# Kernel tuning notes

Hardware: AMD Instinct MI355X
Metric: run time of the kernel (lower is better)

Reference implementation:

```python
import jax, jax.numpy as jnp
import numpy as np

B, D_IN, H, C, K, ND = 65536, 1024, 512, 2, 4, 7
LN_EPS = 1e-5
CE_W = jnp.array([0.1, 0.9], dtype=jnp.float32)


def setup_inputs() -> dict:
    key = jax.random.key(0)
    ks = jax.random.split(key, 12)
    x = jax.random.normal(ks[0], (B, D_IN), dtype=jnp.float32)
    labels = jax.random.randint(ks[1], (B,), 0, C)
    domain = jax.random.randint(ks[2], (B,), 0, ND)
    fc1_w = jax.random.normal(ks[3], (120, D_IN), dtype=jnp.float32) / np.sqrt(D_IN)
    fc1_b = jnp.zeros((120,), dtype=jnp.float32)
    fc2_w = jax.random.normal(ks[4], (H, 120), dtype=jnp.float32) / np.sqrt(120)
    fc2_b = jnp.zeros((H,), dtype=jnp.float32)
    ln_g = jnp.ones((H,), dtype=jnp.float32)
    ln_b = jnp.zeros((H,), dtype=jnp.float32)
    sms = 0.1 * jax.random.normal(ks[5], (K + 1, H, C), dtype=jnp.float32)
    sm_biases = 0.1 * jax.random.normal(ks[6], (K + 1, C), dtype=jnp.float32)
    embs = 1e-4 * jax.random.normal(ks[7], (ND, K), dtype=jnp.float32)
    cs_wt = jnp.asarray(0.1, dtype=jnp.float32) + 1e-4 * jax.random.normal(ks[8], (), dtype=jnp.float32)
    return {"x": x, "labels": labels, "domain": domain, "fc1_w": fc1_w, "fc1_b": fc1_b,
            "fc2_w": fc2_w, "fc2_b": fc2_b, "ln_g": ln_g, "ln_b": ln_b,
            "sms": sms, "sm_biases": sm_biases, "embs": embs, "cs_wt": cs_wt}


def _weighted_ce(logits, labels, w):
    # torch CrossEntropyLoss(weight=w): sum_i w[y_i]*nll_i / sum_i w[y_i]
    logp = jax.nn.log_softmax(logits, axis=-1)
    nll = -jnp.take_along_axis(logp, labels[:, None], axis=1)[:, 0]
    wl = w[labels]
    return jnp.sum(wl * nll) / jnp.sum(wl)


def reference(x, labels, domain, fc1_w, fc1_b, fc2_w, fc2_b, ln_g, ln_b, sms, sm_biases, embs, cs_wt):
    h = jax.nn.relu(x @ fc1_w.T + fc1_b)           # [B,120]
    h = jax.nn.relu(h @ fc2_w.T + fc2_b)           # [B,H]
    mu = jnp.mean(h, axis=-1, keepdims=True)
    var = jnp.var(h, axis=-1, keepdims=True)
    h = (h - mu) / jnp.sqrt(var + LN_EPS) * ln_g + ln_b

    # common classifier (expert 0)
    logits_common = h @ sms[0] + sm_biases[0]      # [B,C]

    # domain mixture weights
    dom1h = jax.nn.one_hot(domain, ND, dtype=jnp.float32)
    c_wts = dom1h @ embs                           # [B,K]
    c_wts = jnp.tanh(jnp.concatenate([jnp.full((h.shape[0], 1), 1.0, jnp.float32) * cs_wt, c_wts], axis=1))  # [B,K+1]

    # reordered einsum chain: K+1 small GEMMs then weighted sum (avoids [B,K+1,H] weight tensor)
    per_k = jnp.einsum('bh,khc->bkc', h, sms)      # [B,K+1,C]
    logits_spec = jnp.einsum('bk,bkc->bc', c_wts, per_k) + c_wts @ sm_biases  # [B,C]

    specific_loss = _weighted_ce(logits_spec, labels, CE_W)
    class_loss = _weighted_ce(logits_common, labels, CE_W)

    # orthogonality penalty: per-class gram of expert weight columns vs identity
    cps = jnp.einsum('khc,jhc->ckj', sms, sms)     # [C,K+1,K+1]
    orth_loss = jnp.mean((cps - jnp.eye(K + 1, dtype=jnp.float32)[None]) ** 2)

    loss = class_loss + specific_loss + orth_loss
    return (loss, logits_common, class_loss, specific_loss, orth_loss)
```

## Files before the change

### kernel.cpp

```cpp
#include <hip/hip_runtime.h>
#include <hip/hip_bf16.h>

typedef __attribute__((ext_vector_type(8))) short short8;
typedef __attribute__((ext_vector_type(4))) float floatx4;
typedef __attribute__((ext_vector_type(8))) unsigned short ushort8;

#define BTOT 65536
#define WS_W1BF   0u
#define WS_W2BF   262144u
#define WS_GBF    393216u
#define WS_CONST  409600u
#define WS_H1BF   524288u
#define WS_PART   17301504u

__device__ __forceinline__ unsigned short f2bf(float f) {
  unsigned u = __float_as_uint(f);
  unsigned r = u + 0x7FFFu + ((u >> 16) & 1u);
  return (unsigned short)(r >> 16);
}

__device__ __forceinline__ void gload16(const void* g, void* l) {
  __builtin_amdgcn_global_load_lds(
      (const __attribute__((address_space(1))) unsigned int*)g,
      (__attribute__((address_space(3))) unsigned int*)l, 16, 0, 0);
}

__global__ __launch_bounds__(256) void k0_prep(
    const float* __restrict__ w1, const float* __restrict__ w2,
    const float* __restrict__ ln_g, const float* __restrict__ ln_b,
    const float* __restrict__ sms, const float* __restrict__ smb,
    const float* __restrict__ embs, const float* __restrict__ cs,
    unsigned char* __restrict__ ws) {
  const int blk = blockIdx.x, tid = threadIdx.x;
  if (blk < 32) {
    for (int g = blk * 256 + tid; g < 16384; g += 32 * 256) {
      int ks = g >> 10, d = g & 1023;
      int n = d >> 3, cp = d & 7, c = cp ^ (n & 7);
      ushort8 u;
      if (n < 120) {
        const float* s = w1 + n * 1024 + ks * 64 + c * 8;
        float4 v0 = *(const float4*)s, v1 = *(const float4*)(s + 4);
        u[0] = f2bf(v0.x); u[1] = f2bf(v0.y); u[2] = f2bf(v0.z); u[3] = f2bf(v0.w);
        u[4] = f2bf(v1.x); u[5] = f2bf(v1.y); u[6] = f2bf(v1.z); u[7] = f2bf(v1.w);
      } else {
#pragma unroll
        for (int j = 0; j < 8; ++j) u[j] = 0;
      }
      *(ushort8*)(ws + WS_W1BF + (unsigned)g * 16) = u;
    }
  } else if (blk < 40) {
    for (int g = (blk - 32) * 256 + tid; g < 8192; g += 8 * 256) {
      int lane = g & 63, f = g >> 6;
      int nt = f & 3, ks = (f >> 2) & 3, w = f >> 4;
      int n = w * 64 + nt * 16 + (lane & 15);
      ushort8 u;
#pragma unroll
      for (int j = 0; j < 8; ++j) {
        int k = ks * 32 + (lane >> 4) * 8 + j;
        u[j] = (k < 120) ? f2bf(w2[n * 120 + k]) : (unsigned short)0;
      }
      *(ushort8*)(ws + WS_W2BF + (unsigned)g * 16) = u;
    }
  } else if (blk == 40) {
    for (int e = tid; e < 1024; e += 256) {
      int t = e >> 6, lane = e & 63, q = lane & 15;
      ushort8 u;
#pragma unroll
      for (int j = 0; j < 8; ++j) {
        int k = t * 32 + (lane >> 4) * 8 + j;
        float v = 0.f;
        if (q < 10) { int kk = q >> 1, c = q & 1; v = ln_g[k] * sms[kk * 1024 + k * 2 + c]; }
        u[j] = f2bf(v);
      }
      *(ushort8*)(ws + WS_GBF + (unsigned)e * 16) = u;
    }
  } else {
    float* cst = (float*)(ws + WS_CONST);
    int lane = tid & 63, w = tid >> 6;
    for (int q = w; q < 10; q += 4) {
      int kk = q >> 1, c = q & 1;
      float s = 0.f;
#pragma unroll
      for (int i = 0; i < 8; ++i) { int k = lane + 64 * i; s += ln_b[k] * sms[kk * 1024 + k * 2 + c]; }
#pragma unroll
      for (int o = 32; o >= 1; o >>= 1) s += __shfl_xor(s, o);
      if (lane == 0) cst[q] = s + smb[kk * 2 + c];
    }
    if (tid == 0) cst[16] = tanhf(cs[0]);
    if (tid < 28) cst[32 + tid] = tanhf(embs[tid]);
  }
}

__global__ __launch_bounds__(512) void k1_gemm1(
    const float* __restrict__ x, const unsigned char* __restrict__ w1bf,
    const float* __restrict__ b1, unsigned char* __restrict__ h1bf) {
  __shared__ unsigned char lds[49152];
  const int tid = threadIdx.x, lane = tid & 63, w = tid >> 6;
  const int l15 = lane & 15, l4 = lane >> 4;
  const long row0 = (long)blockIdx.x * 64;

  const int xr = tid >> 3, xc8 = tid & 7;
  const float* xsrc = x + (row0 + xr) * 1024 + xc8 * 8;
  const unsigned xoff = (unsigned)(xr * 128 + ((xc8 * 16) ^ ((xr & 7) << 4)));
  const unsigned char* wsrc = w1bf + w * 2048 + lane * 16;
  const unsigned wdstoff = 16384u + (unsigned)w * 2048;

  const int col = w * 16 + l15;
  const float bias = (col < 120) ? b1[col] : 0.f;

  floatx4 acc[4];
#pragma unroll
  for (int i = 0; i < 4; ++i) acc[i] = floatx4{0.f, 0.f, 0.f, 0.f};

  float4 v0 = *(const float4*)(xsrc);
  float4 v1 = *(const float4*)(xsrc + 4);
  gload16(wsrc, lds + wdstoff);
  gload16(wsrc + 1024, lds + wdstoff + 1024);
  __builtin_amdgcn_sched_barrier(0);
  {
    ushort8 u;
    u[0] = f2bf(v0.x); u[1] = f2bf(v0.y); u[2] = f2bf(v0.z); u[3] = f2bf(v0.w);
    u[4] = f2bf(v1.x); u[5] = f2bf(v1.y); u[6] = f2bf(v1.z); u[7] = f2bf(v1.w);
    *(ushort8*)(lds + xoff) = u;
  }
  v0 = *(const float4*)(xsrc + 64);
  v1 = *(const float4*)(xsrc + 68);
  __builtin_amdgcn_sched_barrier(0);
  asm volatile("s_waitcnt vmcnt(2) lgkmcnt(0)" ::: "memory");
  __builtin_amdgcn_s_barrier();

  for (int ks = 0; ks < 16; ++ks) {
    const unsigned cur = ks & 1u, nxt = cur ^ 1u;
    if (ks < 15) {
      gload16(wsrc + (ks + 1) * 16384, lds + 16384 + nxt * 16384 + (wdstoff - 16384));
      gload16(wsrc + (ks + 1) * 16384 + 1024, lds + 16384 + nxt * 16384 + (wdstoff - 16384) + 1024);
    }
    __builtin_amdgcn_sched_barrier(0);
    if (ks < 15) {
      ushort8 u;
      u[0] = f2bf(v0.x); u[1] = f2bf(v0.y); u[2] = f2bf(v0.z); u[3] = f2bf(v0.w);
      u[4] = f2bf(v1.x); u[5] = f2bf(v1.y); u[6] = f2bf(v1.z); u[7] = f2bf(v1.w);
      *(ushort8*)(lds + nxt * 8192 + xoff) = u;
    }
    if (ks < 14) {
      v0 = *(const float4*)(xsrc + (ks + 2) * 64);
      v1 = *(const float4*)(xsrc + (ks + 2) * 64 + 4);
    }
    __builtin_amdgcn_sched_barrier(0);
    const unsigned char* Xc = lds + cur * 8192;
    const unsigned char* Wc = lds + 16384 + cur * 16384;
#pragma unroll
    for (int ss = 0; ss < 2; ++ss) {
      short8 a[4];
#pragma unroll
      for (int mt = 0; mt < 4; ++mt) {
        int r = mt * 16 + l15;
        a[mt] = *(const short8*)(Xc + r * 128 + ((ss * 64 + l4 * 16) ^ ((r & 7) << 4)));
      }
      short8 b = *(const short8*)(Wc + col * 128 + ((ss * 64 + l4 * 16) ^ ((col & 7) << 4)));
#pragma unroll
      for (int mt = 0; mt < 4; ++mt)
        acc[mt] = __builtin_amdgcn_mfma_f32_16x16x32_bf16(a[mt], b, acc[mt], 0, 0, 0);
    }
    if (ks < 14) {
      asm volatile("s_waitcnt vmcnt(2) lgkmcnt(0)" ::: "memory");
    } else {
      asm volatile("s_waitcnt vmcnt(0) lgkmcnt(0)" ::: "memory");
    }
    __builtin_amdgcn_s_barrier();
  }

  unsigned char* h1s = lds;
#pragma unroll
  for (int mt = 0; mt < 4; ++mt)
#pragma unroll
    for (int r = 0; r < 4; ++r) {
      int row = mt * 16 + l4 * 4 + r;
      float v = acc[mt][r] + bias;
      v = (col < 120) ? (v > 0.f ? v : 0.f) : 0.f;
      *(unsigned short*)(h1s + row * 256 + ((col * 2) ^ ((row & 7) << 4))) = f2bf(v);
    }
  __syncthreads();
  {
    const unsigned char* s = lds + tid * 32;
    unsigned char* d = h1bf + (long)blockIdx.x * 16384 + tid * 32;
    *(float4*)(d) = *(const float4*)(s);
    *(float4*)(d + 16) = *(const float4*)(s + 16);
  }
}

__global__ __launch_bounds__(512, 4) void k2_fused(
    const unsigned char* __restrict__ h1bf, const unsigned char* __restrict__ w2f,
    const unsigned char* __restrict__ gbf, const float* __restrict__ cst,
    const float* __restrict__ b2, const int* __restrict__ labels,
    const int* __restrict__ domain, float* __restrict__ out,
    float* __restrict__ partials) {
  extern __shared__ unsigned char lds[];
  unsigned char* h1s = lds;
  unsigned char* h2s = lds;
  float* stats = (float*)(lds + 65536);
  float* musig = (float*)(lds + 70656);
  float* Af    = (float*)(lds + 71168);

  const int tid = threadIdx.x, lane = tid & 63, w = tid >> 6;
  const int l15 = lane & 15, l4 = lane >> 4;
  const long row0 = (long)blockIdx.x * 64;
  const int n0 = w * 64;

  {
    const unsigned char* hs = h1bf + (long)blockIdx.x * 16384 + w * 2048 + lane * 16;
    gload16(hs, h1s + w * 2048);
    gload16(hs + 1024, h1s + w * 2048 + 1024);
  }
  float b2v[4];
#pragma unroll
  for (int nt = 0; nt < 4; ++nt) b2v[nt] = b2[n0 + nt * 16 + l15];
  __syncthreads();

  floatx4 acc[4][4];
#pragma unroll
  for (int i = 0; i < 4; ++i)
#pragma unroll
    for (int j = 0; j < 4; ++j) acc[i][j] = floatx4{0.f, 0.f, 0.f, 0.f};
#pragma unroll
  for (int ks = 0; ks < 4; ++ks) {
    short8 a[4], b[4];
#pragma unroll
    for (int nt = 0; nt < 4; ++nt)
      b[nt] = *(const short8*)(w2f + (((w * 4 + ks) * 4 + nt) * 64 + lane) * 16);
#pragma unroll
    for (int mt = 0; mt < 4; ++mt) {
      int r = mt * 16 + l15;
      a[mt] = *(const short8*)(h1s + r * 256 + ((ks * 64 + l4 * 16) ^ ((r & 7) << 4)));
    }
#pragma unroll
    for (int mt = 0; mt < 4; ++mt)
#pragma unroll
      for (int nt = 0; nt < 4; ++nt)
        acc[mt][nt] = __builtin_amdgcn_mfma_f32_16x16x32_bf16(a[mt], b[nt], acc[mt][nt], 0, 0, 0);
  }

#pragma unroll
  for (int mt = 0; mt < 4; ++mt)
#pragma unroll
    for (int nt = 0; nt < 4; ++nt)
#pragma unroll
      for (int r = 0; r < 4; ++r) {
        float v = acc[mt][nt][r] + b2v[nt];
        acc[mt][nt][r] = v > 0.f ? v : 0.f;
      }
#pragma unroll
  for (int mt = 0; mt < 4; ++mt)
#pragma unroll
    for (int r = 0; r < 4; ++r) {
      float s = 0.f, q2 = 0.f;
#pragma unroll
      for (int nt = 0; nt < 4; ++nt) { float v = acc[mt][nt][r]; s += v; q2 += v * v; }
#pragma unroll
      for (int o = 1; o <= 8; o <<= 1) { s += __shfl_xor(s, o); q2 += __shfl_xor(q2, o); }
      if (l15 == 0) {
        int row = mt * 16 + l4 * 4 + r;
        stats[row * 20 + w * 2] = s;
        stats[row * 20 + w * 2 + 1] = q2;
      }
    }
  __syncthreads();

  if (tid < 64) {
    float S = 0.f, Q = 0.f;
#pragma unroll
    for (int j = 0; j < 8; ++j) { S += stats[tid * 20 + j * 2]; Q += stats[tid * 20 + j * 2 + 1]; }
    float mu = S * (1.f / 512.f);
    float var = Q * (1.f / 512.f) - mu * mu;
    musig[tid * 2] = mu;
    musig[tid * 2 + 1] = rsqrtf(var + 1e-5f);
  }
  __syncthreads();

#pragma unroll
  for (int mt = 0; mt < 4; ++mt)
#pragma unroll
    for (int r = 0; r < 4; ++r) {
      int row = mt * 16 + l4 * 4 + r;
      float mu = musig[row * 2], rs = musig[row * 2 + 1];
#pragma unroll
      for (int nt = 0; nt < 4; ++nt) {
        int colc = n0 + nt * 16 + l15;
        float hn = (acc[mt][nt][r] - mu) * rs;
        *(unsigned short*)(h2s + row * 1024 + ((colc * 2) ^ ((row & 7) << 4))) = f2bf(hn);
      }
    }
  __syncthreads();

  if (w < 4) {
    floatx4 a3 = floatx4{0.f, 0.f, 0.f, 0.f};
    int row = w * 16 + l15;
#pragma unroll
    for (int t = 0; t < 16; ++t) {
      short8 aa = *(const short8*)(h2s + row * 1024 + ((t * 64 + l4 * 16) ^ ((row & 7) << 4)));
      short8 bb = *(const short8*)(gbf + t * 1024 + lane * 16);
      a3 = __builtin_amdgcn_mfma_f32_16x16x32_bf16(aa, bb, a3, 0, 0, 0);
    }
#pragma unroll
    for (int reg = 0; reg < 4; ++reg) {
      int orow = w * 16 + l4 * 4 + reg;
      if (l15 < 10) Af[orow * 20 + l15] = a3[reg];
    }
  }
  __syncthreads();

  if (tid < 64) {
    long grow = row0 + tid;
    float pd[10];
#pragma unroll
    for (int q = 0; q < 10; ++q) pd[q] = Af[tid * 20 + q] + cst[q];
    int lab = labels[grow], dm = domain[grow];
    float cw0 = cst[16];
    float ls0 = cw0 * pd[0], ls1 = cw0 * pd[1];
#pragma unroll
    for (int kk = 1; kk < 5; ++kk) {
      float c = cst[32 + dm * 4 + kk - 1];
      ls0 += c * pd[kk * 2];
      ls1 += c * pd[kk * 2 + 1];
    }
    float lc0 = pd[0], lc1 = pd[1];
    *(float2*)(out + 1 + grow * 2) = float2{lc0, lc1};
    float m1 = fmaxf(lc0, lc1), n1 = fminf(lc0, lc1);
    float lse1 = m1 + logf(1.f + expf(n1 - m1));
    float nllc = lse1 - (lab ? lc1 : lc0);
    float m2 = fmaxf(ls0, ls1), n2 = fminf(ls0, ls1);
    float lse2 = m2 + logf(1.f + expf(n2 - m2));
    float nlls = lse2 - (lab ? ls1 : ls0);
    float wl = lab ? 0.9f : 0.1f;
    float wsum = wl, scom = wl * nllc, sspec = wl * nlls;
#pragma unroll
    for (int o = 32; o >= 1; o >>= 1) {
      wsum += __shfl_xor(wsum, o);
      scom += __shfl_xor(scom, o);
      sspec += __shfl_xor(sspec, o);
    }
    if (tid == 0) {
      partials[(long)blockIdx.x * 4] = wsum;
      partials[(long)blockIdx.x * 4 + 1] = scom;
      partials[(long)blockIdx.x * 4 + 2] = sspec;
    }
  }
}

__global__ __launch_bounds__(256) void k3_finalize(
    const float* __restrict__ partials, const float* __restrict__ sms,
    float* __restrict__ out) {
  __shared__ float wsums[4][3];
  __shared__ float ow[4];
  const int tid = threadIdx.x;
  const int lane = tid & 63, wid = tid >> 6;
  float sw = 0.f, sc = 0.f, ss = 0.f;
  for (int i = tid; i < 1024; i += 256) {
    sw += partials[i * 4];
    sc += partials[i * 4 + 1];
    ss += partials[i * 4 + 2];
  }
#pragma unroll
  for (int o = 32; o >= 1; o >>= 1) {
    sw += __shfl_xor(sw, o);
    sc += __shfl_xor(sc, o);
    ss += __shfl_xor(ss, o);
  }
  if (lane == 0) { wsums[wid][0] = sw; wsums[wid][1] = sc; wsums[wid][2] = ss; }

  float osum = 0.f;
  for (int p = wid; p < 50; p += 4) {
    int c = p / 25, kk = (p / 5) % 5, j = p % 5;
    float acc = 0.f;
#pragma unroll
    for (int hh = 0; hh < 8; ++hh) {
      int h = lane + 64 * hh;
      acc += sms[kk * 1024 + h * 2 + c] * sms[j * 1024 + h * 2 + c];
    }
#pragma unroll
    for (int o = 32; o >= 1; o >>= 1) acc += __shfl_xor(acc, o);
    float d = acc - ((kk == j) ? 1.f : 0.f);
    osum += d * d;
  }
  if (lane == 0) ow[wid] = osum;
  __syncthreads();
  if (tid == 0) {
    float SW = 0.f, SC = 0.f, SS = 0.f, OS = 0.f;
    for (int w = 0; w < 4; ++w) {
      SW += wsums[w][0]; SC += wsums[w][1]; SS += wsums[w][2]; OS += ow[w];
    }
    float orth = OS * (1.f / 50.f);
    float cls = SC / SW;
    float spec = SS / SW;
    out[0] = cls + spec + orth;
    out[131073] = cls;
    out[131074] = spec;
    out[131075] = orth;
  }
}

extern "C" void kernel_launch(void* const* d_in, const int* in_sizes, int n_in,
                              void* d_out, int out_size, void* d_ws, size_t ws_size,
                              hipStream_t stream) {
  const float* x      = (const float*)d_in[0];
  const int* labels   = (const int*)d_in[1];
  const int* domain   = (const int*)d_in[2];
  const float* fc1_w  = (const float*)d_in[3];
  const float* fc1_b  = (const float*)d_in[4];
  const float* fc2_w  = (const float*)d_in[5];
  const float* fc2_b  = (const float*)d_in[6];
  const float* ln_g   = (const float*)d_in[7];
  const float* ln_b   = (const float*)d_in[8];
  const float* sms    = (const float*)d_in[9];
  const float* sm_b   = (const float*)d_in[10];
  const float* embs   = (const float*)d_in[11];
  const float* cs_wt  = (const float*)d_in[12];
  float* out = (float*)d_out;
  unsigned char* ws = (unsigned char*)d_ws;

  (void)hipFuncSetAttribute((const void*)k2_fused,
                            hipFuncAttributeMaxDynamicSharedMemorySize, 76800);

  hipLaunchKernelGGL(k0_prep, dim3(42), dim3(256), 0, stream,
                     fc1_w, fc2_w, ln_g, ln_b, sms, sm_b, embs, cs_wt, ws);
  hipLaunchKernelGGL(k1_gemm1, dim3(BTOT / 64), dim3(512), 0, stream,
                     x, ws + WS_W1BF, fc1_b, ws + WS_H1BF);
  hipLaunchKernelGGL(k2_fused, dim3(BTOT / 64), dim3(512), 76800, stream,
                     ws + WS_H1BF, ws + WS_W2BF, ws + WS_GBF,
                     (const float*)(ws + WS_CONST), fc2_b,
                     labels, domain, out, (float*)(ws + WS_PART));
  hipLaunchKernelGGL(k3_finalize, dim3(1), dim3(256), 0, stream,
                     (const float*)(ws + WS_PART), sms, out);
}
```

Measured before the change: 109.9 us.

## Feed GEMM1 A-operand from registers with 128-row tiles and permuted h1 layout

GEMM1 now has each wave load its own 16 rows of x straight into registers and convert them to bf16 MFMA A-fragments with packed conversion. This removes the LDS staging of x, and each block now handles 128 rows with all 8 column tiles per wave. To keep the h1 and h2 writes vectorized, the K dimension of h1 and the H dimension of h2 are permuted, and the fc2 and gain weight prep is reordered to match. The aim is less LDS traffic and fewer barriers in the bandwidth-bound x read, at the cost of more accumulators per wave and permuted-index bookkeeping that must stay consistent.

```diff
diff --git a/kernel.cpp b/kernel.cpp
--- a/kernel.cpp
+++ b/kernel.cpp
@@ -17,6 +17,12 @@
   unsigned u = __float_as_uint(f);
   unsigned r = u + 0x7FFFu + ((u >> 16) & 1u);
   return (unsigned short)(r >> 16);
+}
+
+__device__ __forceinline__ unsigned cvtpk(float lo, float hi) {
+  unsigned r;
+  asm("v_cvt_pk_bf16_f32 %0, %1, %2" : "=v"(r) : "v"(lo), "v"(hi));
+  return r;
 }
 
 __device__ __forceinline__ void gload16(const void* g, void* l) {
@@ -56,8 +62,9 @@
       ushort8 u;
 #pragma unroll
       for (int j = 0; j < 8; ++j) {
-        int k = ks * 32 + (lane >> 4) * 8 + j;
-        u[j] = (k < 120) ? f2bf(w2[n * 120 + k]) : (unsigned short)0;
+        int khat = ks * 32 + (lane >> 4) * 8 + j;
+        int kcol = (khat & 7) * 16 + (khat >> 3);
+        u[j] = (kcol < 120) ? f2bf(w2[n * 120 + kcol]) : (unsigned short)0;
       }
       *(ushort8*)(ws + WS_W2BF + (unsigned)g * 16) = u;
     }
@@ -67,9 +74,10 @@
       ushort8 u;
 #pragma unroll
       for (int j = 0; j < 8; ++j) {
-        int k = t * 32 + (lane >> 4) * 8 + j;
+        int khat = t * 32 + (lane >> 4) * 8 + j;
+        int col = (khat >> 6) * 64 + (khat & 3) * 16 + ((khat >> 2) & 15);
         float v = 0.f;
-        if (q < 10) { int kk = q >> 1, c = q & 1; v = ln_g[k] * sms[kk * 1024 + k * 2 + c]; }
+        if (q < 10) { int kk = q >> 1, c = q & 1; v = ln_g[col] * sms[kk * 1024 + col * 2 + c]; }
         u[j] = f2bf(v);
       }
       *(ushort8*)(ws + WS_GBF + (unsigned)e * 16) = u;
@@ -91,101 +99,114 @@
   }
 }
 
-__global__ __launch_bounds__(512) void k1_gemm1(
+__global__ __launch_bounds__(512, 4) void k1_gemm1(
     const float* __restrict__ x, const unsigned char* __restrict__ w1bf,
     const float* __restrict__ b1, unsigned char* __restrict__ h1bf) {
-  __shared__ unsigned char lds[49152];
+  __shared__ unsigned char lds[32768];
   const int tid = threadIdx.x, lane = tid & 63, w = tid >> 6;
   const int l15 = lane & 15, l4 = lane >> 4;
-  const long row0 = (long)blockIdx.x * 64;
-
-  const int xr = tid >> 3, xc8 = tid & 7;
-  const float* xsrc = x + (row0 + xr) * 1024 + xc8 * 8;
-  const unsigned xoff = (unsigned)(xr * 128 + ((xc8 * 16) ^ ((xr & 7) << 4)));
+
+  float b1v[8];
+#pragma unroll
+  for (int nt = 0; nt < 8; ++nt) {
+    int col = nt * 16 + l15;
+    b1v[nt] = b1[col < 120 ? col : 119];
+  }
+  __builtin_amdgcn_sched_barrier(0);
+
+  const float* xbase = x + ((long)blockIdx.x * 128 + w * 16 + l15) * 1024 + l4 * 8;
   const unsigned char* wsrc = w1bf + w * 2048 + lane * 16;
-  const unsigned wdstoff = 16384u + (unsigned)w * 2048;
-
-  const int col = w * 16 + l15;
-  const float bias = (col < 120) ? b1[col] : 0.f;
-
-  floatx4 acc[4];
-#pragma unroll
-  for (int i = 0; i < 4; ++i) acc[i] = floatx4{0.f, 0.f, 0.f, 0.f};
-
-  float4 v0 = *(const float4*)(xsrc);
-  float4 v1 = *(const float4*)(xsrc + 4);
-  gload16(wsrc, lds + wdstoff);
-  gload16(wsrc + 1024, lds + wdstoff + 1024);
+
+  floatx4 acc[8];
+#pragma unroll
+  for (int i = 0; i < 8; ++i) acc[i] = floatx4{0.f, 0.f, 0.f, 0.f};
+
+  float4 p[2][4];
+  gload16(wsrc, lds + w * 2048);
+  gload16(wsrc + 1024, lds + w * 2048 + 1024);
   __builtin_amdgcn_sched_barrier(0);
+#pragma unroll
+  for (int ss = 0; ss < 2; ++ss) {
+    p[0][ss * 2]     = *(const float4*)(xbase + ss * 32);
+    p[0][ss * 2 + 1] = *(const float4*)(xbase + ss * 32 + 4);
+  }
+#pragma unroll
+  for (int ss = 0; ss < 2; ++ss) {
+    p[1][ss * 2]     = *(const float4*)(xbase + 64 + ss * 32);
+    p[1][ss * 2 + 1] = *(const float4*)(xbase + 64 + ss * 32 + 4);
+  }
+  __builtin_amdgcn_sched_barrier(0);
+  asm volatile("s_waitcnt vmcnt(8)" ::: "memory");
+  __builtin_amdgcn_s_barrier();
+
+#pragma unroll
+  for (int t = 0; t < 16; ++t) {
+    const int cur = t & 1;
+    short8 afr[2];
+#pragma unroll
+    for (int ss = 0; ss < 2; ++ss) {
+      float4 a0 = p[cur][ss * 2], a1 = p[cur][ss * 2 + 1];
+      union { unsigned u[4]; short8 s; } tmp;
+      tmp.u[0] = cvtpk(a0.x, a0.y);
+      tmp.u[1] = cvtpk(a0.z, a0.w);
+      tmp.u[2] = cvtpk(a1.x, a1.y);
+      tmp.u[3] = cvtpk(a1.z, a1.w);
+      afr[ss] = tmp.s;
+    }
+    __builtin_amdgcn_sched_barrier(0);
+    if (t < 15) {
+      gload16(wsrc + (t + 1) * 16384, lds + (cur ^ 1) * 16384 + w * 2048);
+      gload16(wsrc + (t + 1) * 16384 + 1024, lds + (cur ^ 1) * 16384 + w * 2048 + 1024);
+    }
+    __builtin_amdgcn_sched_barrier(0);
+    if (t < 14) {
+#pragma unroll
+      for (int ss = 0; ss < 2; ++ss) {
+        p[cur][ss * 2]     = *(const float4*)(xbase + (t + 2) * 64 + ss * 32);
+        p[cur][ss * 2 + 1] = *(const float4*)(xbase + (t + 2) * 64 + ss * 32 + 4);
+      }
+    }
+    __builtin_amdgcn_sched_barrier(0);
+    const unsigned char* Wc = lds + cur * 16384;
+#pragma unroll
+    for (int ss = 0; ss < 2; ++ss)
+#pragma unroll
+      for (int nt = 0; nt < 8; ++nt) {
+        int n = nt * 16 + l15;
+        short8 b = *(const short8*)(Wc + n * 128 + ((ss * 64 + l4 * 16) ^ ((n & 7) << 4)));
+        acc[nt] = __builtin_amdgcn_mfma_f32_16x16x32_bf16(afr[ss], b, acc[nt], 0, 0, 0);
+      }
+    if (t < 14)       asm volatile("s_waitcnt vmcnt(4) lgkmcnt(0)" ::: "memory");
+    else if (t == 14) asm volatile("s_waitcnt vmcnt(0) lgkmcnt(0)" ::: "memory");
+    else              asm volatile("s_waitcnt lgkmcnt(0)" ::: "memory");
+    __builtin_amdgcn_s_barrier();
+  }
+
+#pragma unroll
+  for (int r = 0; r < 4; ++r) {
+    int row = w * 16 + l4 * 4 + r;
+    float v[8];
+#pragma unroll
+    for (int nt = 0; nt < 8; ++nt) {
+      float t0 = acc[nt][r] + b1v[nt];
+      v[nt] = t0 > 0.f ? t0 : 0.f;
+    }
+    if (l15 >= 8) v[7] = 0.f;
+    union { unsigned u[4]; short8 s; } tmp;
+    tmp.u[0] = cvtpk(v[0], v[1]);
+    tmp.u[1] = cvtpk(v[2], v[3]);
+    tmp.u[2] = cvtpk(v[4], v[5]);
+    tmp.u[3] = cvtpk(v[6], v[7]);
+    *(short8*)(lds + row * 256 + ((l15 * 16) ^ ((row & 7) << 4))) = tmp.s;
+  }
+  __syncthreads();
   {
-    ushort8 u;
-    u[0] = f2bf(v0.x); u[1] = f2bf(v0.y); u[2] = f2bf(v0.z); u[3] = f2bf(v0.w);
-    u[4] = f2bf(v1.x); u[5] = f2bf(v1.y); u[6] = f2bf(v1.z); u[7] = f2bf(v1.w);
-    *(ushort8*)(lds + xoff) = u;
-  }
-  v0 = *(const float4*)(xsrc + 64);
-  v1 = *(const float4*)(xsrc + 68);
-  __builtin_amdgcn_sched_barrier(0);
-  asm volatile("s_waitcnt vmcnt(2) lgkmcnt(0)" ::: "memory");
-  __builtin_amdgcn_s_barrier();
-
-  for (int ks = 0; ks < 16; ++ks) {
-    const unsigned cur = ks & 1u, nxt = cur ^ 1u;
-    if (ks < 15) {
-      gload16(wsrc + (ks + 1) * 16384, lds + 16384 + nxt * 16384 + (wdstoff - 16384));
-      gload16(wsrc + (ks + 1) * 16384 + 1024, lds + 16384 + nxt * 16384 + (wdstoff - 16384) + 1024);
-    }
-    __builtin_amdgcn_sched_barrier(0);
-    if (ks < 15) {
-      ushort8 u;
-      u[0] = f2bf(v0.x); u[1] = f2bf(v0.y); u[2] = f2bf(v0.z); u[3] = f2bf(v0.w);
-      u[4] = f2bf(v1.x); u[5] = f2bf(v1.y); u[6] = f2bf(v1.z); u[7] = f2bf(v1.w);
-      *(ushort8*)(lds + nxt * 8192 + xoff) = u;
-    }
-    if (ks < 14) {
-      v0 = *(const float4*)(xsrc + (ks + 2) * 64);
-      v1 = *(const float4*)(xsrc + (ks + 2) * 64 + 4);
-    }
-    __builtin_amdgcn_sched_barrier(0);
-    const unsigned char* Xc = lds + cur * 8192;
-    const unsigned char* Wc = lds + 16384 + cur * 16384;
-#pragma unroll
-    for (int ss = 0; ss < 2; ++ss) {
-      short8 a[4];
-#pragma unroll
-      for (int mt = 0; mt < 4; ++mt) {
-        int r = mt * 16 + l15;
-        a[mt] = *(const short8*)(Xc + r * 128 + ((ss * 64 + l4 * 16) ^ ((r & 7) << 4)));
-      }
-      short8 b = *(const short8*)(Wc + col * 128 + ((ss * 64 + l4 * 16) ^ ((col & 7) << 4)));
-#pragma unroll
-      for (int mt = 0; mt < 4; ++mt)
-        acc[mt] = __builtin_amdgcn_mfma_f32_16x16x32_bf16(a[mt], b, acc[mt], 0, 0, 0);
-    }
-    if (ks < 14) {
-      asm volatile("s_waitcnt vmcnt(2) lgkmcnt(0)" ::: "memory");
-    } else {
-      asm volatile("s_waitcnt vmcnt(0) lgkmcnt(0)" ::: "memory");
-    }
-    __builtin_amdgcn_s_barrier();
-  }
-
-  unsigned char* h1s = lds;
-#pragma unroll
-  for (int mt = 0; mt < 4; ++mt)
-#pragma unroll
-    for (int r = 0; r < 4; ++r) {
-      int row = mt * 16 + l4 * 4 + r;
-      float v = acc[mt][r] + bias;
-      v = (col < 120) ? (v > 0.f ? v : 0.f) : 0.f;
-      *(unsigned short*)(h1s + row * 256 + ((col * 2) ^ ((row & 7) << 4))) = f2bf(v);
-    }
-  __syncthreads();
-  {
-    const unsigned char* s = lds + tid * 32;
-    unsigned char* d = h1bf + (long)blockIdx.x * 16384 + tid * 32;
-    *(float4*)(d) = *(const float4*)(s);
+    const unsigned char* s = lds + tid * 64;
+    unsigned char* d = h1bf + (long)blockIdx.x * 32768 + tid * 64;
+    *(float4*)(d)      = *(const float4*)(s);
     *(float4*)(d + 16) = *(const float4*)(s + 16);
+    *(float4*)(d + 32) = *(const float4*)(s + 32);
+    *(float4*)(d + 48) = *(const float4*)(s + 48);
   }
 }
 
@@ -208,7 +229,8 @@
   const int n0 = w * 64;
 
   {
-    const unsigned char* hs = h1bf + (long)blockIdx.x * 16384 + w * 2048 + lane * 16;
+    const unsigned char* hs = h1bf + ((long)(blockIdx.x >> 1)) * 32768 +
+                              (blockIdx.x & 1) * 16384 + w * 2048 + lane * 16;
     gload16(hs, h1s + w * 2048);
     gload16(hs + 1024, h1s + w * 2048 + 1024);
   }
@@ -283,12 +305,10 @@
     for (int r = 0; r < 4; ++r) {
       int row = mt * 16 + l4 * 4 + r;
       float mu = musig[row * 2], rs = musig[row * 2 + 1];
-#pragma unroll
-      for (int nt = 0; nt < 4; ++nt) {
-        int colc = n0 + nt * 16 + l15;
-        float hn = (acc[mt][nt][r] - mu) * rs;
-        *(unsigned short*)(h2s + row * 1024 + ((colc * 2) ^ ((row & 7) << 4))) = f2bf(hn);
-      }
+      uint2 qq;
+      qq.x = cvtpk((acc[mt][0][r] - mu) * rs, (acc[mt][1][r] - mu) * rs);
+      qq.y = cvtpk((acc[mt][2][r] - mu) * rs, (acc[mt][3][r] - mu) * rs);
+      *(uint2*)(h2s + row * 1024 + ((w * 128 + l15 * 8) ^ ((row & 7) << 4))) = qq;
     }
   __syncthreads();
 
@@ -423,7 +443,7 @@
 
   hipLaunchKernelGGL(k0_prep, dim3(42), dim3(256), 0, stream,
                      fc1_w, fc2_w, ln_g, ln_b, sms, sm_b, embs, cs_wt, ws);
-  hipLaunchKernelGGL(k1_gemm1, dim3(BTOT / 64), dim3(512), 0, stream,
+  hipLaunchKernelGGL(k1_gemm1, dim3(BTOT / 128), dim3(512), 0, stream,
                      x, ws + WS_W1BF, fc1_b, ws + WS_H1BF);
   hipLaunchKernelGGL(k2_fused, dim3(BTOT / 64), dim3(512), 76800, stream,
                      ws + WS_H1BF, ws + WS_W2BF, ws + WS_GBF,
```

After: 104.7 us. 1.05x faster.
